# Performance work log

Hardware: AMD Instinct MI355X
Metric: run time of the kernel (lower is better)

The kernel has to match this reference:

```python
import jax, jax.numpy as jnp
import numpy as np

C_QKV = 1024
C_HIDDEN = 64
NUM_HEADS = 16
INF = 1e9


def setup_inputs() -> dict:
    key = jax.random.key(0)
    ks = jax.random.split(key, 10)
    B, S = 2, 2048
    d = C_QKV
    hd = C_HIDDEN * NUM_HEADS
    sc = 0.02
    return {
        "input_qkv": jax.random.normal(ks[0], (B, S, d), jnp.float32),
        "mask": jnp.ones((B, 1, 1, S), jnp.float32),
        "bias": jax.random.normal(ks[1], (1, NUM_HEADS, S, S), jnp.float32) * sc,
        "wq": jax.random.normal(ks[2], (d, hd), jnp.float32) * sc,
        "wk": jax.random.normal(ks[3], (d, hd), jnp.float32) * sc,
        "wv": jax.random.normal(ks[4], (d, hd), jnp.float32) * sc,
        "wg": jax.random.normal(ks[5], (d, hd), jnp.float32) * sc,
        "bg": jnp.zeros((hd,), jnp.float32),
        "wo": jax.random.normal(ks[6], (hd, d), jnp.float32) * sc,
        "bo": jnp.zeros((d,), jnp.float32),
    }


def reference(input_qkv, mask, bias, wq, wk, wv, wg, bg, wo, bo):
    B, S, _ = input_qkv.shape
    H, C = NUM_HEADS, C_HIDDEN
    # projections -> [B, H, S, C]
    q = (input_qkv @ wq).reshape(B, S, H, C).transpose(0, 2, 1, 3)
    k = (input_qkv @ wk).reshape(B, S, H, C).transpose(0, 2, 1, 3)
    v = (input_qkv @ wv).reshape(B, S, H, C).transpose(0, 2, 1, 3)
    q = q / jnp.asarray(C, q.dtype) ** 0.5
    # scores [B, H, S, S] with additive mask and pair bias
    a = jnp.einsum("bhqc,bhkc->bhqk", q, k)
    a = a + (mask - 1.0) * INF + bias
    a = jax.nn.softmax(a, axis=-1)
    o = jnp.einsum("bhqk,bhkc->bhqc", a, v).transpose(0, 2, 1, 3)  # [B,S,H,C]
    gate = jax.nn.sigmoid(input_qkv @ wg + bg).reshape(B, S, H, C)
    o = (o * gate).reshape(B, S, H * C)
    return o @ wo + bo
```

## Files before the change

kernel.cpp:

```cpp
#include <hip/hip_runtime.h>
#include <hip/hip_bf16.h>
#include <stdint.h>

typedef unsigned short u16;
typedef __attribute__((ext_vector_type(8))) short short8;
typedef __attribute__((ext_vector_type(4))) short short4v;
typedef __attribute__((ext_vector_type(4))) float f32x4;

#define MFMA16 __builtin_amdgcn_mfma_f32_16x16x32_bf16

#define GLOAD_LDS16(gsrc, ldst) \
  __builtin_amdgcn_global_load_lds((const __attribute__((address_space(1))) void*)(gsrc), \
                                   (__attribute__((address_space(3))) void*)(ldst), 16, 0, 0)

__device__ __forceinline__ u16 f2bf(float x) {
  union { float f; uint32_t u; } v; v.f = x;
  uint32_t r = v.u + 0x7FFFu + ((v.u >> 16) & 1u);
  return (u16)(r >> 16);
}
__device__ __forceinline__ u16 f2bf_rn(float x) {
  __hip_bfloat16 h = __float2bfloat16(x);
  return *reinterpret_cast<u16*>(&h);
}
__device__ __forceinline__ float bf2f(u16 b) {
  union { uint32_t u; float f; } v; v.u = ((uint32_t)b) << 16;
  return v.f;
}

__global__ __launch_bounds__(256) void convert_bf16_kernel(
    const float* __restrict__ in, u16* __restrict__ out, int n) {
  int i = (blockIdx.x * 256 + threadIdx.x) * 8;
  if (i >= n) return;
  float4 a = *(const float4*)(in + i);
  float4 b = *(const float4*)(in + i + 4);
  short8 t;
  t[0] = (short)f2bf(a.x); t[1] = (short)f2bf(a.y);
  t[2] = (short)f2bf(a.z); t[3] = (short)f2bf(a.w);
  t[4] = (short)f2bf(b.x); t[5] = (short)f2bf(b.y);
  t[6] = (short)f2bf(b.z); t[7] = (short)f2bf(b.w);
  *(short8*)(out + i) = t;
}

__global__ __launch_bounds__(256) void transpose_w64_4(
    const float* __restrict__ w0, const float* __restrict__ w1,
    const float* __restrict__ w2, const float* __restrict__ w3,
    u16* __restrict__ WT) {
  __shared__ float tile[64][68];
  const int t = threadIdx.x;
  const int z = blockIdx.z;
  const float* W = (z == 0) ? w0 : (z == 1) ? w1 : (z == 2) ? w2 : w3;
  u16* dst_base = WT + (size_t)z * 1024 * 1024;
  const int k0 = blockIdx.x * 64, n0 = blockIdx.y * 64;
  {
    int r = t >> 2, c0 = (t & 3) * 16;
    const float* src = W + (size_t)(k0 + r) * 1024 + n0 + c0;
#pragma unroll
    for (int j = 0; j < 16; j += 4) {
      float4 v = *(const float4*)(src + j);
      tile[r][c0 + j + 0] = v.x; tile[r][c0 + j + 1] = v.y;
      tile[r][c0 + j + 2] = v.z; tile[r][c0 + j + 3] = v.w;
    }
  }
  __syncthreads();
  {
    int n = t >> 2, kq = (t & 3) * 16;
    short8 t0, t1;
#pragma unroll
    for (int j = 0; j < 8; ++j)  t0[j] = (short)f2bf(tile[kq + j][n]);
#pragma unroll
    for (int j = 0; j < 8; ++j)  t1[j] = (short)f2bf(tile[kq + 8 + j][n]);
    u16* dst = dst_base + (size_t)(n0 + n) * 1024 + k0 + kq;
    *(short8*)dst = t0;
    *(short8*)(dst + 8) = t1;
  }
}

__global__ __launch_bounds__(256) void transpose_w64(
    const float* __restrict__ W, u16* __restrict__ WT, int KK, int NN) {
  __shared__ float tile[64][68];
  const int t = threadIdx.x;
  const int k0 = blockIdx.x * 64, n0 = blockIdx.y * 64;
  {
    int r = t >> 2, c0 = (t & 3) * 16;
    const float* src = W + (size_t)(k0 + r) * NN + n0 + c0;
#pragma unroll
    for (int j = 0; j < 16; j += 4) {
      float4 v = *(const float4*)(src + j);
      tile[r][c0 + j + 0] = v.x; tile[r][c0 + j + 1] = v.y;
      tile[r][c0 + j + 2] = v.z; tile[r][c0 + j + 3] = v.w;
    }
  }
  __syncthreads();
  {
    int n = t >> 2, kq = (t & 3) * 16;
    short8 t0, t1;
#pragma unroll
    for (int j = 0; j < 8; ++j)  t0[j] = (short)f2bf(tile[kq + j][n]);
#pragma unroll
    for (int j = 0; j < 8; ++j)  t1[j] = (short)f2bf(tile[kq + 8 + j][n]);
    u16* dst = WT + (size_t)(n0 + n) * KK + k0 + kq;
    *(short8*)dst = t0;
    *(short8*)(dst + 8) = t1;
  }
}

__global__ __launch_bounds__(256) void transpose_v64(
    const u16* __restrict__ vin, u16* __restrict__ vout) {
  __shared__ u16 tile[64][80];
  const int t = threadIdx.x;
  const int s0 = blockIdx.x * 64;
  const int bh = blockIdx.y;
  const int b = bh >> 4, h = bh & 15;
  {
    int r = t >> 2, c0 = (t & 3) * 16;
    const u16* src = vin + (size_t)(b * 2048 + s0 + r) * 1024 + h * 64 + c0;
    *(short8*)&tile[r][c0] = *(const short8*)src;
    *(short8*)&tile[r][c0 + 8] = *(const short8*)(src + 8);
  }
  __syncthreads();
  {
    int c = t >> 2, s4 = (t & 3) * 16;
    short8 t0, t1;
#pragma unroll
    for (int j = 0; j < 8; ++j) t0[j] = (short)tile[s4 + j][c];
#pragma unroll
    for (int j = 0; j < 8; ++j) t1[j] = (short)tile[s4 + 8 + j][c];
    u16* dst = vout + (size_t)(bh * 64 + c) * 2048 + s0 + s4;
    *(short8*)dst = t0;
    *(short8*)(dst + 8) = t1;
  }
}

__global__ __launch_bounds__(256) void gemm_bt128(
    const u16* __restrict__ A, const u16* __restrict__ BTbase,
    void* __restrict__ dstbase, const float* __restrict__ bvec, int mode) {
  const int K = 1024;
  const int tid = threadIdx.x, lane = tid & 63, w = tid >> 6;
  const int wr = w >> 1, wc = w & 1;
  const int l15 = lane & 15, lg = lane >> 4;
  const int z = (mode < 0) ? (int)blockIdx.z : mode;
  const u16* BT = (mode < 0) ? BTbase + (size_t)z * 1024 * 1024 : BTbase;
  const int rbase = blockIdx.x * 128;
  const int nbase = blockIdx.y * 128;
  __shared__ u16 lsA[128 * 64];
  __shared__ u16 lsB[128 * 64];
  f32x4 acc[4][4] = {};
  const int col8 = (lane & 7) * 8;
  for (int kt = 0; kt < K / 64; ++kt) {
#pragma unroll
    for (int i = 0; i < 4; ++i) {
      int row = w * 32 + i * 8 + (lane >> 3);
      const u16* sa = A + (size_t)(rbase + row) * K + kt * 64 + col8;
      GLOAD_LDS16(sa, lsA + (w * 32 + i * 8) * 64 + lane * 8);
      const u16* sb = BT + (size_t)(nbase + row) * K + kt * 64 + col8;
      GLOAD_LDS16(sb, lsB + (w * 32 + i * 8) * 64 + lane * 8);
    }
    __syncthreads();
#pragma unroll
    for (int kk = 0; kk < 2; ++kk) {
      short8 af[4], bfr[4];
#pragma unroll
      for (int m = 0; m < 4; ++m)
        af[m] = *(const short8*)&lsA[(wr * 64 + m * 16 + l15) * 64 + kk * 32 + lg * 8];
#pragma unroll
      for (int n = 0; n < 4; ++n)
        bfr[n] = *(const short8*)&lsB[(wc * 64 + n * 16 + l15) * 64 + kk * 32 + lg * 8];
#pragma unroll
      for (int m = 0; m < 4; ++m)
#pragma unroll
        for (int n = 0; n < 4; ++n)
          acc[m][n] = MFMA16(af[m], bfr[n], acc[m][n], 0, 0, 0);
    }
    __syncthreads();
  }
  const int r0 = rbase + wr * 64;
  const int c0 = nbase + wc * 64;
  if (z == 4) {
    float* out = (float*)dstbase;
#pragma unroll
    for (int m = 0; m < 4; ++m)
#pragma unroll
      for (int n = 0; n < 4; ++n)
#pragma unroll
        for (int i = 0; i < 4; ++i) {
          int r = r0 + m * 16 + lg * 4 + i;
          int c = c0 + n * 16 + l15;
          out[(size_t)r * 1024 + c] = acc[m][n][i] + bvec[c];
        }
  } else {
    u16* dq = (u16*)dstbase + (size_t)z * 4096 * 1024;
#pragma unroll
    for (int m = 0; m < 4; ++m)
#pragma unroll
      for (int n = 0; n < 4; ++n)
#pragma unroll
        for (int i = 0; i < 4; ++i) {
          int r = r0 + m * 16 + lg * 4 + i;
          int c = c0 + n * 16 + l15;
          float v = acc[m][n][i];
          if (z == 0) v *= 0.125f;
          else if (z == 3) v = 1.f / (1.f + __expf(-(v + bvec[c])));
          dq[(size_t)r * 1024 + c] = f2bf(v);
        }
  }
}

__global__ __launch_bounds__(512, 2) void attn_kernel(
    const u16* __restrict__ qws, const u16* __restrict__ kws,
    const u16* __restrict__ vt, const u16* __restrict__ gws,
    const float* __restrict__ bias, const float* __restrict__ mask,
    u16* __restrict__ og) {
  const int tid = threadIdx.x;
  const int lane = tid & 63;
  const int w = tid >> 6;
  const int bb = w >> 2;
  const int ws = w & 3;
  const int l15 = lane & 15, lg = lane >> 4;
  const int qt = blockIdx.x;
  const int h = blockIdx.y;
  const int kb0 = ((h << 1) | (qt >> 3)) & 31;

#define KWIN(KB) (((KB) + kb0) & 31)

  __shared__ __align__(16) u16 ring[2][16384];
  __shared__ __align__(16) u16 lsB[2][9216];
  __shared__ __align__(16) u16 lsP[8][2304];
  __shared__ __align__(16) u16 lsM[4096];

  const float* bias_base = bias + ((size_t)h * 2048 + qt * 128) * 2048;
  const u16* k_base0 = kws + (size_t)h * 64;
  const u16* k_base1 = kws + (size_t)2048 * 1024 + h * 64;
  const u16* vt_base0 = vt + (size_t)(h * 64) * 2048;
  const u16* vt_base1 = vt + (size_t)((16 + h) * 64) * 2048;

  {
    float4 m0 = *(const float4*)(mask + tid * 8);
    float4 m1 = *(const float4*)(mask + tid * 8 + 4);
    short8 mm;
    mm[0] = (short)f2bf((m0.x - 1.f) * 1e9f); mm[1] = (short)f2bf((m0.y - 1.f) * 1e9f);
    mm[2] = (short)f2bf((m0.z - 1.f) * 1e9f); mm[3] = (short)f2bf((m0.w - 1.f) * 1e9f);
    mm[4] = (short)f2bf((m1.x - 1.f) * 1e9f); mm[5] = (short)f2bf((m1.y - 1.f) * 1e9f);
    mm[6] = (short)f2bf((m1.z - 1.f) * 1e9f); mm[7] = (short)f2bf((m1.w - 1.f) * 1e9f);
    *(short8*)&lsM[tid * 8] = mm;
  }

  const size_t qrow0 = (size_t)(bb * 2048 + qt * 128 + ws * 32 + l15) * 1024 + h * 64;
  const size_t qrow1 = qrow0 + 16 * 1024;
  short8 qf00 = *(const short8*)(qws + qrow0 + lg * 8);
  short8 qf01 = *(const short8*)(qws + qrow0 + 32 + lg * 8);
  short8 qf10 = *(const short8*)(qws + qrow1 + lg * 8);
  short8 qf11 = *(const short8*)(qws + qrow1 + 32 + lg * 8);
  asm volatile("" :: "v"(qf00), "v"(qf01), "v"(qf10), "v"(qf11));
  asm volatile("s_waitcnt vmcnt(0)" ::: "memory");
  __builtin_amdgcn_sched_barrier(0);

  f32x4 O[2][4] = {};
  float lacc0 = 0.f, lacc1 = 0.f;
  f32x4 kX0, kX1, vX0, vX1, kY0, kY1, vY0, vY1;
  f32x4 bX0, bX1, bX2, bX3, bY0, bY1, bY2, bY3;

#define STAGE_ISSUE(K0, K1, V0, V1, KB) {                                           \
    int kw_ = KWIN(KB);                                                             \
    int r_ = tid >> 3, cg_ = tid & 7;                                               \
    const u16* kp0 = k_base0 + (size_t)(kw_ * 64 + r_) * 1024 + cg_ * 8;            \
    const u16* kp1 = k_base1 + (size_t)(kw_ * 64 + r_) * 1024 + cg_ * 8;            \
    const u16* vp0 = vt_base0 + (size_t)r_ * 2048 + kw_ * 64 + cg_ * 8;             \
    const u16* vp1 = vt_base1 + (size_t)r_ * 2048 + kw_ * 64 + cg_ * 8;             \
    asm volatile("global_load_dwordx4 %0, %1, off" : "=v"(K0) : "v"(kp0));          \
    asm volatile("global_load_dwordx4 %0, %1, off" : "=v"(K1) : "v"(kp1));          \
    asm volatile("global_load_dwordx4 %0, %1, off" : "=v"(V0) : "v"(vp0));          \
    asm volatile("global_load_dwordx4 %0, %1, off" : "=v"(V1) : "v"(vp1));          \
  }

#define STAGE_WRITE(SLOT, K0, K1, V0, V1) {                                         \
    int r_ = tid >> 3, cg_ = tid & 7;                                               \
    int d0_ = (r_ * 8 + (cg_ ^ (r_ & 7))) * 8;                                      \
    *(f32x4*)&ring[SLOT][d0_] = K0;                                                 \
    *(f32x4*)&ring[SLOT][4096 + d0_] = V0;                                          \
    *(f32x4*)&ring[SLOT][8192 + d0_] = K1;                                          \
    *(f32x4*)&ring[SLOT][12288 + d0_] = V1;                                         \
  }

#define BIAS_ISSUE(R0, R1, R2, R3, KB) {                                            \
    const float* bp_ = bias_base + (size_t)(tid >> 2) * 2048 + KWIN(KB) * 64 +      \
                       (tid & 3) * 4;                                               \
    asm volatile("global_load_dwordx4 %0, %1, off" : "=v"(R0) : "v"(bp_));          \
    asm volatile("global_load_dwordx4 %0, %1, off" : "=v"(R1) : "v"(bp_ + 16));     \
    asm volatile("global_load_dwordx4 %0, %1, off" : "=v"(R2) : "v"(bp_ + 32));     \
    asm volatile("global_load_dwordx4 %0, %1, off" : "=v"(R3) : "v"(bp_ + 48));     \
  }

#define BIAS_WRITE(SLOT, R0, R1, R2, R3) {                                          \
    int row_ = tid >> 2, c0_ = (tid & 3) * 4;                                       \
    u16* d_ = &lsB[SLOT][row_ * 72 + c0_];                                          \
    short4v p0_, p1_, p2_, p3_;                                                     \
    _Pragma("unroll") for (int i = 0; i < 4; ++i) {                                 \
      p0_[i] = (short)f2bf_rn(R0[i]); p1_[i] = (short)f2bf_rn(R1[i]);               \
      p2_[i] = (short)f2bf_rn(R2[i]); p3_[i] = (short)f2bf_rn(R3[i]);               \
    }                                                                               \
    *(short4v*)&d_[0] = p0_;  *(short4v*)&d_[16] = p1_;                             \
    *(short4v*)&d_[32] = p2_; *(short4v*)&d_[48] = p3_;                             \
  }

#define COMPUTE(SLOT, KB) {                                                         \
    const u16* Kc_ = &ring[SLOT][bb * 8192];                                        \
    const u16* Vc_ = &ring[SLOT][bb * 8192 + 4096];                                 \
    f32x4 s_[2][4];                                                                 \
    _Pragma("unroll") for (int kt = 0; kt < 4; ++kt) {                              \
      int krow_ = kt * 16 + l15;                                                    \
      int sw_ = krow_ & 7;                                                          \
      short8 kfa_ = *(const short8*)&Kc_[(krow_ * 8 + (lg ^ sw_)) * 8];             \
      short8 kfb_ = *(const short8*)&Kc_[(krow_ * 8 + ((4 + lg) ^ sw_)) * 8];       \
      short4v mk_ = *(const short4v*)&lsM[bb * 2048 + KWIN(KB) * 64 + kt * 16 + lg * 4]; \
      short4v bv0_ = *(const short4v*)&lsB[SLOT][(ws * 32 + l15) * 72 + kt * 16 + lg * 4]; \
      short4v bv1_ = *(const short4v*)&lsB[SLOT][(ws * 32 + 16 + l15) * 72 + kt * 16 + lg * 4]; \
      f32x4 ci0_, ci1_;                                                             \
      _Pragma("unroll") for (int i = 0; i < 4; ++i) {                               \
        float m_ = bf2f((u16)mk_[i]);                                               \
        ci0_[i] = bf2f((u16)bv0_[i]) + m_;                                          \
        ci1_[i] = bf2f((u16)bv1_[i]) + m_;                                          \
      }                                                                             \
      s_[0][kt] = MFMA16(kfa_, qf00, ci0_, 0, 0, 0);                                \
      s_[0][kt] = MFMA16(kfb_, qf01, s_[0][kt], 0, 0, 0);                           \
      s_[1][kt] = MFMA16(kfa_, qf10, ci1_, 0, 0, 0);                                \
      s_[1][kt] = MFMA16(kfb_, qf11, s_[1][kt], 0, 0, 0);                           \
    }                                                                               \
    _Pragma("unroll") for (int kt = 0; kt < 4; ++kt) {                              \
      short4v p0_, p1_;                                                             \
      _Pragma("unroll") for (int i = 0; i < 4; ++i) {                               \
        float e0_ = __expf(s_[0][kt][i]); lacc0 += e0_; p0_[i] = (short)f2bf_rn(e0_); \
        float e1_ = __expf(s_[1][kt][i]); lacc1 += e1_; p1_[i] = (short)f2bf_rn(e1_); \
      }                                                                             \
      *(short4v*)&lsP[w][(l15) * 72 + kt * 16 + lg * 4] = p0_;                      \
      *(short4v*)&lsP[w][(16 + l15) * 72 + kt * 16 + lg * 4] = p1_;                 \
    }                                                                               \
    short8 pf00_ = *(const short8*)&lsP[w][(l15) * 72 + lg * 8];                    \
    short8 pf01_ = *(const short8*)&lsP[w][(l15) * 72 + 32 + lg * 8];               \
    short8 pf10_ = *(const short8*)&lsP[w][(16 + l15) * 72 + lg * 8];               \
    short8 pf11_ = *(const short8*)&lsP[w][(16 + l15) * 72 + 32 + lg * 8];          \
    _Pragma("unroll") for (int cf = 0; cf < 4; ++cf) {                              \
      int c_ = cf * 16 + l15;                                                       \
      int sw_ = c_ & 7;                                                             \
      short8 vf0_ = *(const short8*)&Vc_[(c_ * 8 + (lg ^ sw_)) * 8];                \
      short8 vf1_ = *(const short8*)&Vc_[(c_ * 8 + ((4 + lg) ^ sw_)) * 8];          \
      O[0][cf] = MFMA16(vf0_, pf00_, O[0][cf], 0, 0, 0);                            \
      O[0][cf] = MFMA16(vf1_, pf01_, O[0][cf], 0, 0, 0);                            \
      O[1][cf] = MFMA16(vf0_, pf10_, O[1][cf], 0, 0, 0);                            \
      O[1][cf] = MFMA16(vf1_, pf11_, O[1][cf], 0, 0, 0);                            \
    } }

#define BODY(KB, N, ISK0, ISK1, ISV0, ISV1, IB0, IB1, IB2, IB3,                     \
             WRK0, WRK1, WRV0, WRV1, WB0, WB1, WB2, WB3) {                          \
    if ((KB) + 2 < 32) {                                                            \
      STAGE_ISSUE(ISK0, ISK1, ISV0, ISV1, (KB) + 2);                                \
      BIAS_ISSUE(IB0, IB1, IB2, IB3, (KB) + 2);                                     \
    }                                                                               \
    COMPUTE((KB) & 1, KB);                                                          \
    asm volatile("s_waitcnt vmcnt(" #N ")" ::: "memory");                           \
    __builtin_amdgcn_sched_barrier(0);                                              \
    if ((KB) + 1 < 32) {                                                            \
      STAGE_WRITE(((KB) + 1) & 1, WRK0, WRK1, WRV0, WRV1);                          \
      BIAS_WRITE(((KB) + 1) & 1, WB0, WB1, WB2, WB3);                               \
      asm volatile("s_waitcnt lgkmcnt(0)" ::: "memory");                            \
      __builtin_amdgcn_sched_barrier(0);                                            \
      __builtin_amdgcn_s_barrier();                                                 \
    } }

  STAGE_ISSUE(kX0, kX1, vX0, vX1, 0);
  BIAS_ISSUE(bX0, bX1, bX2, bX3, 0);
  STAGE_ISSUE(kY0, kY1, vY0, vY1, 1);
  BIAS_ISSUE(bY0, bY1, bY2, bY3, 1);
  asm volatile("s_waitcnt vmcnt(8)" ::: "memory");
  __builtin_amdgcn_sched_barrier(0);
  STAGE_WRITE(0, kX0, kX1, vX0, vX1);
  BIAS_WRITE(0, bX0, bX1, bX2, bX3);
  asm volatile("s_waitcnt lgkmcnt(0)" ::: "memory");
  __builtin_amdgcn_sched_barrier(0);
  __builtin_amdgcn_s_barrier();

  for (int kb2 = 0; kb2 < 30; kb2 += 2) {
    BODY(kb2,     8, kX0, kX1, vX0, vX1, bX0, bX1, bX2, bX3,
         kY0, kY1, vY0, vY1, bY0, bY1, bY2, bY3);
    BODY(kb2 + 1, 8, kY0, kY1, vY0, vY1, bY0, bY1, bY2, bY3,
         kX0, kX1, vX0, vX1, bX0, bX1, bX2, bX3);
  }
  BODY(30, 0, kX0, kX1, vX0, vX1, bX0, bX1, bX2, bX3,
       kY0, kY1, vY0, vY1, bY0, bY1, bY2, bY3);
  BODY(31, 0, kY0, kY1, vY0, vY1, bY0, bY1, bY2, bY3,
       kX0, kX1, vX0, vX1, bX0, bX1, bX2, bX3);

  lacc0 += __shfl_xor(lacc0, 16); lacc0 += __shfl_xor(lacc0, 32);
  lacc1 += __shfl_xor(lacc1, 16); lacc1 += __shfl_xor(lacc1, 32);
  {
    float inv0 = 1.f / lacc0, inv1 = 1.f / lacc1;
#pragma unroll
    for (int cf = 0; cf < 4; ++cf) {
      short4v ga = *(const short4v*)(gws + qrow0 + cf * 16 + lg * 4);
      short4v gb = *(const short4v*)(gws + qrow1 + cf * 16 + lg * 4);
      short4v oa, ob;
#pragma unroll
      for (int i = 0; i < 4; ++i) {
        oa[i] = (short)f2bf_rn(O[0][cf][i] * inv0 * bf2f((u16)ga[i]));
        ob[i] = (short)f2bf_rn(O[1][cf][i] * inv1 * bf2f((u16)gb[i]));
      }
      *(short4v*)(og + qrow0 + cf * 16 + lg * 4) = oa;
      *(short4v*)(og + qrow1 + cf * 16 + lg * 4) = ob;
    }
  }
#undef STAGE_ISSUE
#undef STAGE_WRITE
#undef BIAS_ISSUE
#undef BIAS_WRITE
#undef COMPUTE
#undef BODY
#undef KWIN
}

extern "C" void kernel_launch(void* const* d_in, const int* in_sizes, int n_in,
                              void* d_out, int out_size, void* d_ws, size_t ws_size,
                              hipStream_t stream) {
  const float* x    = (const float*)d_in[0];
  const float* mask = (const float*)d_in[1];
  const float* bias = (const float*)d_in[2];
  const float* wq   = (const float*)d_in[3];
  const float* wk   = (const float*)d_in[4];
  const float* wv   = (const float*)d_in[5];
  const float* wg   = (const float*)d_in[6];
  const float* bg   = (const float*)d_in[7];
  const float* wo   = (const float*)d_in[8];
  const float* bo   = (const float*)d_in[9];
  float* out = (float*)d_out;

  char* ws = (char*)d_ws;
  const size_t MB = 1ull << 20;
  u16* xb   = (u16*)(ws + 0);
  u16* wt   = (u16*)(ws + 8 * MB);
  u16* wot  = (u16*)(ws + 16 * MB);
  u16* proj = (u16*)(ws + 18 * MB);
  u16* vtp  = (u16*)(ws + 50 * MB);
  u16* og   = (u16*)(ws + 58 * MB);
  const size_t PSZ = (size_t)4096 * 1024;

  convert_bf16_kernel<<<2048, 256, 0, stream>>>(x, xb, 4096 * 1024);

  transpose_w64_4<<<dim3(16, 16, 4), 256, 0, stream>>>(wq, wk, wv, wg, wt);
  transpose_w64<<<dim3(16, 16), 256, 0, stream>>>(wo, wot, 1024, 1024);

  gemm_bt128<<<dim3(32, 8, 4), 256, 0, stream>>>(xb, wt, (void*)proj, bg, -1);

  transpose_v64<<<dim3(32, 32), 256, 0, stream>>>(proj + 2 * PSZ, vtp);

  attn_kernel<<<dim3(16, 16), 512, 0, stream>>>(proj, proj + PSZ, vtp, proj + 3 * PSZ,
                                                bias, mask, og);

  gemm_bt128<<<dim3(32, 8, 1), 256, 0, stream>>>(og, wot, (void*)out, bo, 4);
}
```

Before: 190.9 us.

## Split attention blocks per batch with 64-query tiles and 256 threads

The attention kernel moves from 256 blocks of 512 threads, each covering 128 queries for both batch elements, to 1024 blocks of 256 threads, each covering 64 queries of a single batch element. Each warp now owns 16 query rows instead of 32, and the LDS buffers shrink to match. The intent is finer-grained scheduling and more resident blocks per CU. The cost is that the pair bias tile is no longer shared across the two batch elements inside one block, so it is fetched twice and relies on L2 hits from neighbouring blocks. Each K/V fragment read from LDS also feeds half as many MFMAs.

```diff
diff --git a/kernel.cpp b/kernel.cpp
--- a/kernel.cpp
+++ b/kernel.cpp
@@ -205,7 +205,7 @@
   }
 }
 
-__global__ __launch_bounds__(512, 2) void attn_kernel(
+__global__ __launch_bounds__(256, 2) void attn_kernel(
     const u16* __restrict__ qws, const u16* __restrict__ kws,
     const u16* __restrict__ vt, const u16* __restrict__ gws,
     const float* __restrict__ bias, const float* __restrict__ mask,
@@ -213,29 +213,28 @@
   const int tid = threadIdx.x;
   const int lane = tid & 63;
   const int w = tid >> 6;
-  const int bb = w >> 2;
-  const int ws = w & 3;
   const int l15 = lane & 15, lg = lane >> 4;
-  const int qt = blockIdx.x;
-  const int h = blockIdx.y;
-  const int kb0 = ((h << 1) | (qt >> 3)) & 31;
+  const int bx = blockIdx.x;
+  const int qt = bx >> 5;
+  const int rem = bx & 31;
+  const int h = rem >> 1;
+  const int bb = rem & 1;
+  const int kb0 = ((h << 1) | (qt >> 4)) & 31;
 
 #define KWIN(KB) (((KB) + kb0) & 31)
 
-  __shared__ __align__(16) u16 ring[2][16384];
-  __shared__ __align__(16) u16 lsB[2][9216];
-  __shared__ __align__(16) u16 lsP[8][2304];
-  __shared__ __align__(16) u16 lsM[4096];
-
-  const float* bias_base = bias + ((size_t)h * 2048 + qt * 128) * 2048;
-  const u16* k_base0 = kws + (size_t)h * 64;
-  const u16* k_base1 = kws + (size_t)2048 * 1024 + h * 64;
-  const u16* vt_base0 = vt + (size_t)(h * 64) * 2048;
-  const u16* vt_base1 = vt + (size_t)((16 + h) * 64) * 2048;
-
-  {
-    float4 m0 = *(const float4*)(mask + tid * 8);
-    float4 m1 = *(const float4*)(mask + tid * 8 + 4);
+  __shared__ __align__(16) u16 ring[2][8192];
+  __shared__ __align__(16) u16 lsB[2][4608];
+  __shared__ __align__(16) u16 lsP[4][1152];
+  __shared__ __align__(16) u16 lsM[2048];
+
+  const float* bias_base = bias + ((size_t)h * 2048 + qt * 64) * 2048;
+  const u16* k_base = kws + (size_t)(bb * 2048) * 1024 + h * 64;
+  const u16* vt_base = vt + (size_t)((bb * 16 + h) * 64) * 2048;
+
+  {
+    float4 m0 = *(const float4*)(mask + bb * 2048 + tid * 8);
+    float4 m1 = *(const float4*)(mask + bb * 2048 + tid * 8 + 4);
     short8 mm;
     mm[0] = (short)f2bf((m0.x - 1.f) * 1e9f); mm[1] = (short)f2bf((m0.y - 1.f) * 1e9f);
     mm[2] = (short)f2bf((m0.z - 1.f) * 1e9f); mm[3] = (short)f2bf((m0.w - 1.f) * 1e9f);
@@ -244,41 +243,37 @@
     *(short8*)&lsM[tid * 8] = mm;
   }
 
-  const size_t qrow0 = (size_t)(bb * 2048 + qt * 128 + ws * 32 + l15) * 1024 + h * 64;
-  const size_t qrow1 = qrow0 + 16 * 1024;
-  short8 qf00 = *(const short8*)(qws + qrow0 + lg * 8);
-  short8 qf01 = *(const short8*)(qws + qrow0 + 32 + lg * 8);
-  short8 qf10 = *(const short8*)(qws + qrow1 + lg * 8);
-  short8 qf11 = *(const short8*)(qws + qrow1 + 32 + lg * 8);
-  asm volatile("" :: "v"(qf00), "v"(qf01), "v"(qf10), "v"(qf11));
+  const size_t qrow = (size_t)(bb * 2048 + qt * 64 + w * 16 + l15) * 1024 + h * 64;
+  short8 qf0 = *(const short8*)(qws + qrow + lg * 8);
+  short8 qf1 = *(const short8*)(qws + qrow + 32 + lg * 8);
+  asm volatile("" :: "v"(qf0), "v"(qf1));
   asm volatile("s_waitcnt vmcnt(0)" ::: "memory");
   __builtin_amdgcn_sched_barrier(0);
 
-  f32x4 O[2][4] = {};
-  float lacc0 = 0.f, lacc1 = 0.f;
+  f32x4 O[4] = {};
+  float lacc = 0.f;
   f32x4 kX0, kX1, vX0, vX1, kY0, kY1, vY0, vY1;
   f32x4 bX0, bX1, bX2, bX3, bY0, bY1, bY2, bY3;
 
 #define STAGE_ISSUE(K0, K1, V0, V1, KB) {                                           \
     int kw_ = KWIN(KB);                                                             \
-    int r_ = tid >> 3, cg_ = tid & 7;                                               \
-    const u16* kp0 = k_base0 + (size_t)(kw_ * 64 + r_) * 1024 + cg_ * 8;            \
-    const u16* kp1 = k_base1 + (size_t)(kw_ * 64 + r_) * 1024 + cg_ * 8;            \
-    const u16* vp0 = vt_base0 + (size_t)r_ * 2048 + kw_ * 64 + cg_ * 8;             \
-    const u16* vp1 = vt_base1 + (size_t)r_ * 2048 + kw_ * 64 + cg_ * 8;             \
-    asm volatile("global_load_dwordx4 %0, %1, off" : "=v"(K0) : "v"(kp0));          \
-    asm volatile("global_load_dwordx4 %0, %1, off" : "=v"(K1) : "v"(kp1));          \
-    asm volatile("global_load_dwordx4 %0, %1, off" : "=v"(V0) : "v"(vp0));          \
-    asm volatile("global_load_dwordx4 %0, %1, off" : "=v"(V1) : "v"(vp1));          \
+    int r_ = tid >> 2, cg_ = tid & 3;                                               \
+    const u16* kp_ = k_base + (size_t)(kw_ * 64 + r_) * 1024 + cg_ * 8;             \
+    const u16* vp_ = vt_base + (size_t)r_ * 2048 + kw_ * 64 + cg_ * 8;              \
+    asm volatile("global_load_dwordx4 %0, %1, off" : "=v"(K0) : "v"(kp_));          \
+    asm volatile("global_load_dwordx4 %0, %1, off" : "=v"(K1) : "v"(kp_ + 32));     \
+    asm volatile("global_load_dwordx4 %0, %1, off" : "=v"(V0) : "v"(vp_));          \
+    asm volatile("global_load_dwordx4 %0, %1, off" : "=v"(V1) : "v"(vp_ + 32));     \
   }
 
 #define STAGE_WRITE(SLOT, K0, K1, V0, V1) {                                         \
-    int r_ = tid >> 3, cg_ = tid & 7;                                               \
+    int r_ = tid >> 2, cg_ = tid & 3;                                               \
     int d0_ = (r_ * 8 + (cg_ ^ (r_ & 7))) * 8;                                      \
+    int d1_ = (r_ * 8 + ((4 + cg_) ^ (r_ & 7))) * 8;                                \
     *(f32x4*)&ring[SLOT][d0_] = K0;                                                 \
+    *(f32x4*)&ring[SLOT][d1_] = K1;                                                 \
     *(f32x4*)&ring[SLOT][4096 + d0_] = V0;                                          \
-    *(f32x4*)&ring[SLOT][8192 + d0_] = K1;                                          \
-    *(f32x4*)&ring[SLOT][12288 + d0_] = V1;                                         \
+    *(f32x4*)&ring[SLOT][4096 + d1_] = V1;                                          \
   }
 
 #define BIAS_ISSUE(R0, R1, R2, R3, KB) {                                            \
@@ -303,50 +298,38 @@
   }
 
 #define COMPUTE(SLOT, KB) {                                                         \
-    const u16* Kc_ = &ring[SLOT][bb * 8192];                                        \
-    const u16* Vc_ = &ring[SLOT][bb * 8192 + 4096];                                 \
-    f32x4 s_[2][4];                                                                 \
+    const u16* Kc_ = &ring[SLOT][0];                                                \
+    const u16* Vc_ = &ring[SLOT][4096];                                             \
+    f32x4 s_[4];                                                                    \
     _Pragma("unroll") for (int kt = 0; kt < 4; ++kt) {                              \
       int krow_ = kt * 16 + l15;                                                    \
       int sw_ = krow_ & 7;                                                          \
       short8 kfa_ = *(const short8*)&Kc_[(krow_ * 8 + (lg ^ sw_)) * 8];             \
       short8 kfb_ = *(const short8*)&Kc_[(krow_ * 8 + ((4 + lg) ^ sw_)) * 8];       \
-      short4v mk_ = *(const short4v*)&lsM[bb * 2048 + KWIN(KB) * 64 + kt * 16 + lg * 4]; \
-      short4v bv0_ = *(const short4v*)&lsB[SLOT][(ws * 32 + l15) * 72 + kt * 16 + lg * 4]; \
-      short4v bv1_ = *(const short4v*)&lsB[SLOT][(ws * 32 + 16 + l15) * 72 + kt * 16 + lg * 4]; \
-      f32x4 ci0_, ci1_;                                                             \
-      _Pragma("unroll") for (int i = 0; i < 4; ++i) {                               \
-        float m_ = bf2f((u16)mk_[i]);                                               \
-        ci0_[i] = bf2f((u16)bv0_[i]) + m_;                                          \
-        ci1_[i] = bf2f((u16)bv1_[i]) + m_;                                          \
-      }                                                                             \
-      s_[0][kt] = MFMA16(kfa_, qf00, ci0_, 0, 0, 0);                                \
-      s_[0][kt] = MFMA16(kfb_, qf01, s_[0][kt], 0, 0, 0);                           \
-      s_[1][kt] = MFMA16(kfa_, qf10, ci1_, 0, 0, 0);                                \
-      s_[1][kt] = MFMA16(kfb_, qf11, s_[1][kt], 0, 0, 0);                           \
+      short4v mk_ = *(const short4v*)&lsM[KWIN(KB) * 64 + kt * 16 + lg * 4];        \
+      short4v bv_ = *(const short4v*)&lsB[SLOT][(w * 16 + l15) * 72 + kt * 16 + lg * 4]; \
+      f32x4 ci_;                                                                    \
+      _Pragma("unroll") for (int i = 0; i < 4; ++i)                                 \
+        ci_[i] = bf2f((u16)bv_[i]) + bf2f((u16)mk_[i]);                             \
+      s_[kt] = MFMA16(kfa_, qf0, ci_, 0, 0, 0);                                     \
+      s_[kt] = MFMA16(kfb_, qf1, s_[kt], 0, 0, 0);                                  \
     }                                                                               \
     _Pragma("unroll") for (int kt = 0; kt < 4; ++kt) {                              \
-      short4v p0_, p1_;                                                             \
+      short4v p_;                                                                   \
       _Pragma("unroll") for (int i = 0; i < 4; ++i) {                               \
-        float e0_ = __expf(s_[0][kt][i]); lacc0 += e0_; p0_[i] = (short)f2bf_rn(e0_); \
-        float e1_ = __expf(s_[1][kt][i]); lacc1 += e1_; p1_[i] = (short)f2bf_rn(e1_); \
+        float e_ = __expf(s_[kt][i]); lacc += e_; p_[i] = (short)f2bf_rn(e_);       \
       }                                                                             \
-      *(short4v*)&lsP[w][(l15) * 72 + kt * 16 + lg * 4] = p0_;                      \
-      *(short4v*)&lsP[w][(16 + l15) * 72 + kt * 16 + lg * 4] = p1_;                 \
+      *(short4v*)&lsP[w][l15 * 72 + kt * 16 + lg * 4] = p_;                         \
     }                                                                               \
-    short8 pf00_ = *(const short8*)&lsP[w][(l15) * 72 + lg * 8];                    \
-    short8 pf01_ = *(const short8*)&lsP[w][(l15) * 72 + 32 + lg * 8];               \
-    short8 pf10_ = *(const short8*)&lsP[w][(16 + l15) * 72 + lg * 8];               \
-    short8 pf11_ = *(const short8*)&lsP[w][(16 + l15) * 72 + 32 + lg * 8];          \
+    short8 pf0_ = *(const short8*)&lsP[w][l15 * 72 + lg * 8];                       \
+    short8 pf1_ = *(const short8*)&lsP[w][l15 * 72 + 32 + lg * 8];                  \
     _Pragma("unroll") for (int cf = 0; cf < 4; ++cf) {                              \
       int c_ = cf * 16 + l15;                                                       \
       int sw_ = c_ & 7;                                                             \
       short8 vf0_ = *(const short8*)&Vc_[(c_ * 8 + (lg ^ sw_)) * 8];                \
       short8 vf1_ = *(const short8*)&Vc_[(c_ * 8 + ((4 + lg) ^ sw_)) * 8];          \
-      O[0][cf] = MFMA16(vf0_, pf00_, O[0][cf], 0, 0, 0);                            \
-      O[0][cf] = MFMA16(vf1_, pf01_, O[0][cf], 0, 0, 0);                            \
-      O[1][cf] = MFMA16(vf0_, pf10_, O[1][cf], 0, 0, 0);                            \
-      O[1][cf] = MFMA16(vf1_, pf11_, O[1][cf], 0, 0, 0);                            \
+      O[cf] = MFMA16(vf0_, pf0_, O[cf], 0, 0, 0);                                   \
+      O[cf] = MFMA16(vf1_, pf1_, O[cf], 0, 0, 0);                                   \
     } }
 
 #define BODY(KB, N, ISK0, ISK1, ISV0, ISV1, IB0, IB1, IB2, IB3,                     \
@@ -389,22 +372,18 @@
   BODY(31, 0, kY0, kY1, vY0, vY1, bY0, bY1, bY2, bY3,
        kX0, kX1, vX0, vX1, bX0, bX1, bX2, bX3);
 
-  lacc0 += __shfl_xor(lacc0, 16); lacc0 += __shfl_xor(lacc0, 32);
-  lacc1 += __shfl_xor(lacc1, 16); lacc1 += __shfl_xor(lacc1, 32);
-  {
-    float inv0 = 1.f / lacc0, inv1 = 1.f / lacc1;
+  lacc += __shfl_xor(lacc, 16);
+  lacc += __shfl_xor(lacc, 32);
+  {
+    float inv = 1.f / lacc;
 #pragma unroll
     for (int cf = 0; cf < 4; ++cf) {
-      short4v ga = *(const short4v*)(gws + qrow0 + cf * 16 + lg * 4);
-      short4v gb = *(const short4v*)(gws + qrow1 + cf * 16 + lg * 4);
-      short4v oa, ob;
-#pragma unroll
-      for (int i = 0; i < 4; ++i) {
-        oa[i] = (short)f2bf_rn(O[0][cf][i] * inv0 * bf2f((u16)ga[i]));
-        ob[i] = (short)f2bf_rn(O[1][cf][i] * inv1 * bf2f((u16)gb[i]));
-      }
-      *(short4v*)(og + qrow0 + cf * 16 + lg * 4) = oa;
-      *(short4v*)(og + qrow1 + cf * 16 + lg * 4) = ob;
+      short4v ga = *(const short4v*)(gws + qrow + cf * 16 + lg * 4);
+      short4v oa;
+#pragma unroll
+      for (int i = 0; i < 4; ++i)
+        oa[i] = (short)f2bf_rn(O[cf][i] * inv * bf2f((u16)ga[i]));
+      *(short4v*)(og + qrow + cf * 16 + lg * 4) = oa;
     }
   }
 #undef STAGE_ISSUE
@@ -450,8 +429,8 @@
 
   transpose_v64<<<dim3(32, 32), 256, 0, stream>>>(proj + 2 * PSZ, vtp);
 
-  attn_kernel<<<dim3(16, 16), 512, 0, stream>>>(proj, proj + PSZ, vtp, proj + 3 * PSZ,
-                                                bias, mask, og);
+  attn_kernel<<<1024, 256, 0, stream>>>(proj, proj + PSZ, vtp, proj + 3 * PSZ,
+                                        bias, mask, og);
 
   gemm_bt128<<<dim3(32, 8, 1), 256, 0, stream>>>(og, wot, (void*)out, bo, 4);
 }
```

Result: slower. 220.7 us (+15.6%).
